# Optimization experiments

Hardware: AMD Instinct MI355X
Metric: run time of the kernel (lower is better)

Reference implementation:

```python
import jax, jax.numpy as jnp
import numpy as np

B, S, D, H = 2, 2048, 1024, 16
HD = D // H  # head dim = 64; scale uses sqrt(d_k/num_heads) = sqrt(D/H) since d_k==d_model


def setup_inputs() -> dict:
    key = jax.random.key(0)
    ks = jax.random.split(key, 12)
    s = 1.0 / np.sqrt(D)
    inp = {
        "Q": jax.random.normal(ks[0], (B, S, D), jnp.float32),
        "K": jax.random.normal(ks[1], (B, S, D), jnp.float32),
        "V": jax.random.normal(ks[2], (B, S, D), jnp.float32),
        "mask": jnp.tril(jnp.ones((S, S), jnp.int32))[None, None],  # [1,1,S,S] causal
        "Wq": jax.random.normal(ks[3], (D, D), jnp.float32) * s,
        "bq": jnp.zeros((D,), jnp.float32),
        "Wk": jax.random.normal(ks[4], (D, D), jnp.float32) * s,
        "bk": jnp.zeros((D,), jnp.float32),
        "Wv": jax.random.normal(ks[5], (D, D), jnp.float32) * s,
        "bv": jnp.zeros((D,), jnp.float32),
        "Wo": jax.random.normal(ks[6], (D, D), jnp.float32) * s,
        "bo": jnp.zeros((D,), jnp.float32),
    }
    return inp


def _split_heads(x):
    # [B,S,D] -> [B,H,S,HD]
    b, s, _ = x.shape
    return x.reshape(b, s, H, HD).transpose(0, 2, 1, 3)


def reference(Q, K, V, mask, Wq, bq, Wk, bk, Wv, bv, Wo, bo):
    q = _split_heads(Q @ Wq.T + bq)
    k = _split_heads(K @ Wk.T + bk)
    v = _split_heads(V @ Wv.T + bv)
    scale = 1.0 / jnp.sqrt(jnp.asarray(D / H, q.dtype))  # d_k/num_heads with d_k=d_model
    scores = jnp.einsum('bhqd,bhkd->bhqk', q, k) * scale
    scores = jnp.where(mask == 0, jnp.asarray(-1e9, scores.dtype), scores)
    probs = jax.nn.softmax(scores, axis=-1)
    z = jnp.einsum('bhqk,bhkd->bhqd', probs, v)  # [B,H,S,HD]
    z = z.transpose(0, 2, 1, 3).reshape(Q.shape[0], Q.shape[1], D)
    return z @ Wo.T + bo
```

## Files before the change

kernel.cpp:

```cpp
#include <hip/hip_runtime.h>
#include <hip/hip_bf16.h>

typedef unsigned short u16;
typedef unsigned int u32;
typedef __attribute__((ext_vector_type(8))) short s16x8;
typedef __attribute__((ext_vector_type(4))) float f32x4;
typedef __attribute__((ext_vector_type(16))) float f32x16;

#define NB 2
#define NH 16
#define NS 2048
#define ND 1024
#define QSCALE 0.1803368801111244f

#define AS1(p) ((const __attribute__((address_space(1))) void*)(p))
#define AS3(p) ((__attribute__((address_space(3))) void*)(p))

__device__ __forceinline__ u16 f2bf(float f) {
  u32 u = __float_as_uint(f);
  u = u + 0x7FFFu + ((u >> 16) & 1u);
  return (u16)(u >> 16);
}

__device__ __forceinline__ u32 pkbf(float a, float b) {
  __hip_bfloat162 h = __float22bfloat162_rn(make_float2(a, b));
  union { __hip_bfloat162 h; u32 u; } cv;
  cv.h = h;
  return cv.u;
}

__global__ __launch_bounds__(256) void cvt_kernel(
    const float* __restrict__ q, const float* __restrict__ k,
    const float* __restrict__ v, const float* __restrict__ wq,
    const float* __restrict__ wk, const float* __restrict__ wv,
    const float* __restrict__ wo, u16* __restrict__ Xbf,
    u16* __restrict__ Wbf) {
  const int z = blockIdx.z;
  const float* src;
  u16* dst;
  size_t n;
  const size_t NX = (size_t)4096 * 1024, NW = (size_t)1024 * 1024;
  if (z == 0)      { src = q;  dst = Xbf;          n = NX; }
  else if (z == 1) { src = k;  dst = Xbf + NX;     n = NX; }
  else if (z == 2) { src = v;  dst = Xbf + 2 * NX; n = NX; }
  else if (z == 3) { src = wq; dst = Wbf;          n = NW; }
  else if (z == 4) { src = wk; dst = Wbf + NW;     n = NW; }
  else if (z == 5) { src = wv; dst = Wbf + 2 * NW; n = NW; }
  else             { src = wo; dst = Wbf + 3 * NW; n = NW; }
  const size_t n4 = n >> 2;
  for (size_t i = (size_t)blockIdx.x * 256 + threadIdx.x; i < n4;
       i += (size_t)gridDim.x * 256) {
    float4 a = ((const float4*)src)[i];
    uint2 p;
    p.x = (u32)f2bf(a.x) | ((u32)f2bf(a.y) << 16);
    p.y = (u32)f2bf(a.z) | ((u32)f2bf(a.w) << 16);
    ((uint2*)dst)[i] = p;
  }
}

__global__ __launch_bounds__(256) void gemm_qkv_fast(
    const u16* __restrict__ Xbf, const u16* __restrict__ Wbf,
    const float* __restrict__ bq, const float* __restrict__ bk,
    const float* __restrict__ bv, u16* __restrict__ qh, u16* __restrict__ kh,
    u16* __restrict__ vT) {
  const int which = blockIdx.z;
  const u16* A = Xbf + (size_t)which * 4096 * 1024;
  const u16* B = Wbf + (size_t)which * 1024 * 1024;
  const float* bias = (which == 0) ? bq : (which == 1) ? bk : bv;
  const int m0 = blockIdx.y * 128, n0 = blockIdx.x * 128;
  const int tid = threadIdx.x;
  const int w = tid >> 6, l = tid & 63, lr = l & 15, lg = l >> 4;
  const int wr = (w >> 1) * 64, wc = (w & 1) * 64;

  __shared__ u16 As[128 * 32];
  __shared__ u16 Bs[128 * 32];

  const f32x4 fzero = {0.f, 0.f, 0.f, 0.f};
  f32x4 acc[4][4];
#pragma unroll
  for (int m = 0; m < 4; ++m)
#pragma unroll
    for (int n = 0; n < 4; ++n) acc[m][n] = fzero;

  for (int k0 = 0; k0 < 1024; k0 += 32) {
#pragma unroll
    for (int i = 0; i < 2; ++i) {
      int c = i * 256 + tid;
      int row = c >> 2, k4 = (c & 3) ^ (row & 3);
      const u16* sa = A + (size_t)(m0 + row) * 1024 + k0 + k4 * 8;
      const u16* sb = B + (size_t)(n0 + row) * 1024 + k0 + k4 * 8;
      u16* da = As + (i * 256 + w * 64) * 8;
      u16* db = Bs + (i * 256 + w * 64) * 8;
      __builtin_amdgcn_global_load_lds(AS1(sa), AS3(da), 16, 0, 0);
      __builtin_amdgcn_global_load_lds(AS1(sb), AS3(db), 16, 0, 0);
    }
    __syncthreads();
    s16x8 af[4], bf[4];
#pragma unroll
    for (int m = 0; m < 4; ++m) {
      int row = wr + m * 16 + lr;
      af[m] = *(const s16x8*)(As + row * 32 + ((lg ^ (row & 3)) * 8));
    }
#pragma unroll
    for (int n = 0; n < 4; ++n) {
      int row = wc + n * 16 + lr;
      bf[n] = *(const s16x8*)(Bs + row * 32 + ((lg ^ (row & 3)) * 8));
    }
#pragma unroll
    for (int m = 0; m < 4; ++m)
#pragma unroll
      for (int n = 0; n < 4; ++n)
        acc[m][n] = __builtin_amdgcn_mfma_f32_16x16x32_bf16(af[m], bf[n],
                                                            acc[m][n], 0, 0, 0);
    __syncthreads();
  }

#pragma unroll
  for (int m = 0; m < 4; ++m) {
#pragma unroll
    for (int n = 0; n < 4; ++n) {
#pragma unroll
      for (int i = 0; i < 4; ++i) {
        int row = m0 + wr + m * 16 + 4 * lg + i;
        int col = n0 + wc + n * 16 + lr;
        float val = acc[m][n][i] + bias[col];
        if (which == 0) val *= QSCALE;
        int bbi = row >> 11, ss = row & 2047;
        int hhd = col >> 6, hd = col & 63;
        if (which == 0) {
          qh[(((size_t)bbi * NH + hhd) * NS + ss) * 64 + hd] = f2bf(val);
        } else if (which == 1) {
          kh[(((size_t)bbi * NH + hhd) * NS + ss) * 64 + hd] = f2bf(val);
        } else {
          vT[(((size_t)bbi * NH + hhd) * 64 + hd) * NS + ss] = f2bf(val);
        }
      }
    }
  }
}

__global__ __launch_bounds__(256) void gemm_out_fast(
    const u16* __restrict__ zin, const u16* __restrict__ Wbf,
    const float* __restrict__ bo, float* __restrict__ out) {
  const u16* B = Wbf + (size_t)3 * 1024 * 1024;
  const int m0 = blockIdx.y * 128, n0 = blockIdx.x * 128;
  const int tid = threadIdx.x;
  const int w = tid >> 6, l = tid & 63, lr = l & 15, lg = l >> 4;
  const int wr = (w >> 1) * 64, wc = (w & 1) * 64;

  __shared__ u16 As[128 * 32];
  __shared__ u16 Bs[128 * 32];

  const f32x4 fzero = {0.f, 0.f, 0.f, 0.f};
  f32x4 acc[4][4];
#pragma unroll
  for (int m = 0; m < 4; ++m)
#pragma unroll
    for (int n = 0; n < 4; ++n) acc[m][n] = fzero;

  for (int k0 = 0; k0 < 1024; k0 += 32) {
#pragma unroll
    for (int i = 0; i < 2; ++i) {
      int c = i * 256 + tid;
      int row = c >> 2, k4 = (c & 3) ^ (row & 3);
      const u16* sa = zin + (size_t)(m0 + row) * 1024 + k0 + k4 * 8;
      const u16* sb = B + (size_t)(n0 + row) * 1024 + k0 + k4 * 8;
      u16* da = As + (i * 256 + w * 64) * 8;
      u16* db = Bs + (i * 256 + w * 64) * 8;
      __builtin_amdgcn_global_load_lds(AS1(sa), AS3(da), 16, 0, 0);
      __builtin_amdgcn_global_load_lds(AS1(sb), AS3(db), 16, 0, 0);
    }
    __syncthreads();
    s16x8 af[4], bf[4];
#pragma unroll
    for (int m = 0; m < 4; ++m) {
      int row = wr + m * 16 + lr;
      af[m] = *(const s16x8*)(As + row * 32 + ((lg ^ (row & 3)) * 8));
    }
#pragma unroll
    for (int n = 0; n < 4; ++n) {
      int row = wc + n * 16 + lr;
      bf[n] = *(const s16x8*)(Bs + row * 32 + ((lg ^ (row & 3)) * 8));
    }
#pragma unroll
    for (int m = 0; m < 4; ++m)
#pragma unroll
      for (int n = 0; n < 4; ++n)
        acc[m][n] = __builtin_amdgcn_mfma_f32_16x16x32_bf16(af[m], bf[n],
                                                            acc[m][n], 0, 0, 0);
    __syncthreads();
  }

#pragma unroll
  for (int m = 0; m < 4; ++m)
#pragma unroll
    for (int n = 0; n < 4; ++n)
#pragma unroll
      for (int i = 0; i < 4; ++i) {
        int row = m0 + wr + m * 16 + 4 * lg + i;
        int col = n0 + wc + n * 16 + lr;
        out[(size_t)row * 1024 + col] = acc[m][n][i] + bo[col];
      }
}

__global__ __launch_bounds__(256) void proj_qkv_kernel(
    const float* __restrict__ Qin, const float* __restrict__ Kin,
    const float* __restrict__ Vin,
    const float* __restrict__ Wq, const float* __restrict__ bq,
    const float* __restrict__ Wk, const float* __restrict__ bk,
    const float* __restrict__ Wv, const float* __restrict__ bv,
    u16* __restrict__ qh, u16* __restrict__ kh, u16* __restrict__ vT) {
  const int which = blockIdx.z;
  const float* X = (which == 0) ? Qin : (which == 1) ? Kin : Vin;
  const float* W = (which == 0) ? Wq : (which == 1) ? Wk : Wv;
  const float* bias = (which == 0) ? bq : (which == 1) ? bk : bv;

  const int m0 = blockIdx.y * 128, n0 = blockIdx.x * 128;
  const int tid = threadIdx.x;
  const int w = tid >> 6, l = tid & 63, lr = l & 15, lg = l >> 4;
  const int wr = (w >> 1) * 64, wc = (w & 1) * 64;

  __shared__ u16 As[128][40];
  __shared__ u16 Bs[128][40];

  const f32x4 fzero = {0.f, 0.f, 0.f, 0.f};
  f32x4 acc[4][4];
#pragma unroll
  for (int m = 0; m < 4; ++m)
#pragma unroll
    for (int n = 0; n < 4; ++n) acc[m][n] = fzero;

  for (int k0 = 0; k0 < 1024; k0 += 32) {
#pragma unroll
    for (int i = 0; i < 4; ++i) {
      int idx = tid + i * 256;
      int row = idx >> 3, c4 = (idx & 7) * 4;
      float4 a = *(const float4*)(X + (size_t)(m0 + row) * 1024 + k0 + c4);
      *(u32*)&As[row][c4]     = (u32)f2bf(a.x) | ((u32)f2bf(a.y) << 16);
      *(u32*)&As[row][c4 + 2] = (u32)f2bf(a.z) | ((u32)f2bf(a.w) << 16);
      float4 b = *(const float4*)(W + (size_t)(n0 + row) * 1024 + k0 + c4);
      *(u32*)&Bs[row][c4]     = (u32)f2bf(b.x) | ((u32)f2bf(b.y) << 16);
      *(u32*)&Bs[row][c4 + 2] = (u32)f2bf(b.z) | ((u32)f2bf(b.w) << 16);
    }
    __syncthreads();
    s16x8 af[4], bf[4];
#pragma unroll
    for (int m = 0; m < 4; ++m)
      af[m] = *(const s16x8*)&As[wr + m * 16 + lr][lg * 8];
#pragma unroll
    for (int n = 0; n < 4; ++n)
      bf[n] = *(const s16x8*)&Bs[wc + n * 16 + lr][lg * 8];
#pragma unroll
    for (int m = 0; m < 4; ++m)
#pragma unroll
      for (int n = 0; n < 4; ++n)
        acc[m][n] = __builtin_amdgcn_mfma_f32_16x16x32_bf16(af[m], bf[n],
                                                            acc[m][n], 0, 0, 0);
    __syncthreads();
  }

  u16* dst01 = (which == 0) ? qh : kh;
#pragma unroll
  for (int m = 0; m < 4; ++m) {
#pragma unroll
    for (int n = 0; n < 4; ++n) {
#pragma unroll
      for (int i = 0; i < 4; ++i) {
        int row = m0 + wr + m * 16 + 4 * lg + i;
        int col = n0 + wc + n * 16 + lr;
        float val = acc[m][n][i] + bias[col];
        if (which == 0) val *= QSCALE;
        int bbi = row >> 11, ss = row & 2047;
        int hhd = col >> 6, hd = col & 63;
        if (which < 2) {
          dst01[(((size_t)bbi * NH + hhd) * NS + ss) * 64 + hd] = f2bf(val);
        } else {
          vT[(((size_t)bbi * NH + hhd) * 64 + hd) * NS + ss] = f2bf(val);
        }
      }
    }
  }
}

__global__ __launch_bounds__(256) void proj_out_kernel(
    const u16* __restrict__ zin, const float* __restrict__ Wo,
    const float* __restrict__ bo, float* __restrict__ out) {
  const int m0 = blockIdx.y * 128, n0 = blockIdx.x * 128;
  const int tid = threadIdx.x;
  const int w = tid >> 6, l = tid & 63, lr = l & 15, lg = l >> 4;
  const int wr = (w >> 1) * 64, wc = (w & 1) * 64;

  __shared__ u16 As[128][40];
  __shared__ u16 Bs[128][40];

  const f32x4 fzero = {0.f, 0.f, 0.f, 0.f};
  f32x4 acc[4][4];
#pragma unroll
  for (int m = 0; m < 4; ++m)
#pragma unroll
    for (int n = 0; n < 4; ++n) acc[m][n] = fzero;

  for (int k0 = 0; k0 < 1024; k0 += 32) {
#pragma unroll
    for (int i = 0; i < 2; ++i) {
      int idx = tid + i * 256;
      int row = idx >> 2, c8 = (idx & 3) * 8;
      *(s16x8*)&As[row][c8] =
          *(const s16x8*)(zin + (size_t)(m0 + row) * 1024 + k0 + c8);
    }
#pragma unroll
    for (int i = 0; i < 4; ++i) {
      int idx = tid + i * 256;
      int row = idx >> 3, c4 = (idx & 7) * 4;
      float4 b = *(const float4*)(Wo + (size_t)(n0 + row) * 1024 + k0 + c4);
      *(u32*)&Bs[row][c4]     = (u32)f2bf(b.x) | ((u32)f2bf(b.y) << 16);
      *(u32*)&Bs[row][c4 + 2] = (u32)f2bf(b.z) | ((u32)f2bf(b.w) << 16);
    }
    __syncthreads();
    s16x8 af[4], bf[4];
#pragma unroll
    for (int m = 0; m < 4; ++m)
      af[m] = *(const s16x8*)&As[wr + m * 16 + lr][lg * 8];
#pragma unroll
    for (int n = 0; n < 4; ++n)
      bf[n] = *(const s16x8*)&Bs[wc + n * 16 + lr][lg * 8];
#pragma unroll
    for (int m = 0; m < 4; ++m)
#pragma unroll
      for (int n = 0; n < 4; ++n)
        acc[m][n] = __builtin_amdgcn_mfma_f32_16x16x32_bf16(af[m], bf[n],
                                                            acc[m][n], 0, 0, 0);
    __syncthreads();
  }

#pragma unroll
  for (int m = 0; m < 4; ++m)
#pragma unroll
    for (int n = 0; n < 4; ++n)
#pragma unroll
      for (int i = 0; i < 4; ++i) {
        int row = m0 + wr + m * 16 + 4 * lg + i;
        int col = n0 + wc + n * 16 + lr;
        out[(size_t)row * 1024 + col] = acc[m][n][i] + bo[col];
      }
}

__global__ __launch_bounds__(256) void attn_kernel(
    const u16* __restrict__ qh, const u16* __restrict__ kh,
    const u16* __restrict__ vT, u16* __restrict__ z) {
  const int f = blockIdx.x;
  const int bh = f & 31;
  const int j = f >> 5;
  const int qb = (j < 8) ? (15 - j) : (j - 8);
  const int bb = bh >> 4, hh = bh & 15;
  const int tid = threadIdx.x;
  const int w = tid >> 6, l = tid & 63;
  const int ql = l & 31, hi = l >> 5, hi8 = hi * 8;
  const int q0b = qb * 128;
  const int q0w = q0b + w * 32;

  __shared__ u16 smem[2][2][64][64];

  s16x8 qf[4];
  {
    const u16* qp = qh + ((size_t)bh * NS + q0w + ql) * 64 + hi8;
#pragma unroll
    for (int st = 0; st < 4; ++st) qf[st] = *(const s16x8*)(qp + st * 16);
  }

  f32x16 o0 = {0, 0, 0, 0, 0, 0, 0, 0, 0, 0, 0, 0, 0, 0, 0, 0};
  f32x16 o1 = {0, 0, 0, 0, 0, 0, 0, 0, 0, 0, 0, 0, 0, 0, 0, 0};
  float m_run = -1e30f, l_run = 0.f;

  const int ntiles = (q0b + 128) >> 6;

#pragma unroll
  for (int i = 0; i < 2; ++i) {
    int c = i * 256 + tid;
    int row = c >> 3, k8 = (c & 7) ^ (row & 7);
    const u16* sk = kh + ((size_t)bh * NS + row) * 64 + k8 * 8;
    const u16* sv = vT + ((size_t)bh * 64 + row) * NS + k8 * 8;
    u16* dk = &smem[0][0][0][0] + (i * 256 + w * 64) * 8;
    u16* dv = &smem[0][1][0][0] + (i * 256 + w * 64) * 8;
    __builtin_amdgcn_global_load_lds(AS1(sk), AS3(dk), 16, 0, 0);
    __builtin_amdgcn_global_load_lds(AS1(sv), AS3(dv), 16, 0, 0);
  }
  __syncthreads();

  for (int t = 0; t < ntiles; ++t) {
    if (t + 1 < ntiles) {
      int b1 = (t + 1) & 1;
#pragma unroll
      for (int i = 0; i < 2; ++i) {
        int c = i * 256 + tid;
        int row = c >> 3, k8 = (c & 7) ^ (row & 7);
        const u16* sk =
            kh + ((size_t)bh * NS + (t + 1) * 64 + row) * 64 + k8 * 8;
        const u16* sv =
            vT + ((size_t)bh * 64 + row) * NS + (t + 1) * 64 + k8 * 8;
        u16* dk = &smem[b1][0][0][0] + (i * 256 + w * 64) * 8;
        u16* dv = &smem[b1][1][0][0] + (i * 256 + w * 64) * 8;
        __builtin_amdgcn_global_load_lds(AS1(sk), AS3(dk), 16, 0, 0);
        __builtin_amdgcn_global_load_lds(AS1(sv), AS3(dv), 16, 0, 0);
      }
    }
    const u16* kp = &smem[t & 1][0][0][0];
    const u16* vp = &smem[t & 1][1][0][0];

#pragma unroll
    for (int sub = 0; sub < 2; ++sub) {
      const int kvg = t * 64 + sub * 32;
      if (kvg > q0w) continue;
      const bool masked = (kvg == q0w);

      const int kr = sub * 32 + ql;
      f32x16 s = {0, 0, 0, 0, 0, 0, 0, 0, 0, 0, 0, 0, 0, 0, 0, 0};
#pragma unroll
      for (int st = 0; st < 4; ++st) {
        s16x8 ak = *(const s16x8*)(kp + kr * 64 +
                                   (((st * 2 + hi) ^ (kr & 7)) * 8));
        s = __builtin_amdgcn_mfma_f32_32x32x16_bf16(ak, qf[st], s, 0, 0, 0);
      }

      float sv_[16];
#pragma unroll
      for (int r = 0; r < 16; ++r) {
        float x = s[r];
        if (masked) {
          int kvloc = (r & 3) + 8 * (r >> 2) + 4 * hi;
          if (kvloc > ql) x = -1e30f;
        }
        sv_[r] = x;
      }

      float mx = sv_[0];
#pragma unroll
      for (int r = 1; r < 16; ++r) mx = fmaxf(mx, sv_[r]);
      mx = fmaxf(mx, __shfl_xor(mx, 32, 64));

      if (__any(mx > m_run)) {
        float mnew = fmaxf(m_run, mx);
        float fs = __builtin_amdgcn_exp2f(m_run - mnew);
#pragma unroll
        for (int r = 0; r < 16; ++r) {
          o0[r] *= fs;
          o1[r] *= fs;
        }
        l_run *= fs;
        m_run = mnew;
      }

      float ps = 0.f;
      u32 pk[8];
#pragma unroll
      for (int tt = 0; tt < 8; ++tt) {
        float a = __builtin_amdgcn_exp2f(sv_[2 * tt] - m_run);
        float b = __builtin_amdgcn_exp2f(sv_[2 * tt + 1] - m_run);
        ps += a + b;
        pk[tt] = pkbf(a, b);
      }
      ps += __shfl_xor(ps, 32, 64);
      l_run += ps;

      u32 qk[8];
#pragma unroll
      for (int tt = 0; tt < 8; ++tt) qk[tt] = __shfl_xor(pk[tt], 32, 64);

      union { u32 u[4]; s16x8 h; } pf0, pf1;
      pf0.u[0] = hi ? qk[2] : pk[0];
      pf0.u[1] = hi ? qk[3] : pk[1];
      pf0.u[2] = hi ? pk[2] : qk[0];
      pf0.u[3] = hi ? pk[3] : qk[1];
      pf1.u[0] = hi ? qk[6] : pk[4];
      pf1.u[1] = hi ? qk[7] : pk[5];
      pf1.u[2] = hi ? pk[6] : qk[4];
      pf1.u[3] = hi ? pk[7] : qk[5];

#pragma unroll
      for (int k2 = 0; k2 < 2; ++k2) {
        s16x8 pa = (k2 == 0) ? pf0.h : pf1.h;
        int ch = sub * 4 + k2 * 2 + hi;
        s16x8 av0 = *(const s16x8*)(vp + ql * 64 + ((ch ^ (ql & 7)) * 8));
        s16x8 av1 =
            *(const s16x8*)(vp + (32 + ql) * 64 + ((ch ^ (ql & 7)) * 8));
        o0 = __builtin_amdgcn_mfma_f32_32x32x16_bf16(av0, pa, o0, 0, 0, 0);
        o1 = __builtin_amdgcn_mfma_f32_32x32x16_bf16(av1, pa, o1, 0, 0, 0);
      }
    }
    __syncthreads();
  }

  float inv = 1.f / l_run;
  u16* Zw = &smem[0][0][0][0] + w * (32 * 72);
#pragma unroll
  for (int r = 0; r < 16; r += 2) {
    int d0 = (r & 3) + 8 * (r >> 2) + 4 * hi;
    *(u32*)&Zw[ql * 72 + d0]      = pkbf(o0[r] * inv, o0[r + 1] * inv);
    *(u32*)&Zw[ql * 72 + 32 + d0] = pkbf(o1[r] * inv, o1[r + 1] * inv);
  }
#pragma unroll
  for (int i = 0; i < 4; ++i) {
    int cid = i * 64 + l;
    int row = cid >> 3, c8 = (cid & 7) * 8;
    s16x8 vv = *(const s16x8*)&Zw[row * 72 + c8];
    *(s16x8*)(z + ((size_t)bb * NS + q0w + row) * ND + hh * 64 + c8) = vv;
  }
}

extern "C" void kernel_launch(void* const* d_in, const int* in_sizes, int n_in,
                              void* d_out, int out_size, void* d_ws,
                              size_t ws_size, hipStream_t stream) {
  const float* Q = (const float*)d_in[0];
  const float* K = (const float*)d_in[1];
  const float* V = (const float*)d_in[2];
  const float* Wq = (const float*)d_in[4];
  const float* bq = (const float*)d_in[5];
  const float* Wk = (const float*)d_in[6];
  const float* bk = (const float*)d_in[7];
  const float* Wv = (const float*)d_in[8];
  const float* bv = (const float*)d_in[9];
  const float* Wo = (const float*)d_in[10];
  const float* bo = (const float*)d_in[11];
  float* out = (float*)d_out;

  const size_t M1 = (size_t)1024 * 1024;
  u16* base = (u16*)d_ws;

  if (ws_size >= (size_t)58720256) {
    u16* Wbf = base;
    u16* qh = base + 4 * M1;
    u16* kh = base + 8 * M1;
    u16* vT = base + 12 * M1;
    u16* Xbf = base + 16 * M1;
    u16* zz = base + 16 * M1;

    cvt_kernel<<<dim3(512, 1, 7), 256, 0, stream>>>(Q, K, V, Wq, Wk, Wv, Wo,
                                                    Xbf, Wbf);
    gemm_qkv_fast<<<dim3(8, 32, 3), 256, 0, stream>>>(Xbf, Wbf, bq, bk, bv, qh,
                                                      kh, vT);
    attn_kernel<<<dim3(512), 256, 0, stream>>>(qh, kh, vT, zz);
    gemm_out_fast<<<dim3(8, 32), 256, 0, stream>>>(zz, Wbf, bo, out);
  } else {
    u16* qh = base;
    u16* kh = base + 4 * M1;
    u16* vT = base + 8 * M1;
    u16* zz = base + 12 * M1;
    proj_qkv_kernel<<<dim3(8, 32, 3), 256, 0, stream>>>(Q, K, V, Wq, bq, Wk,
                                                        bk, Wv, bv, qh, kh, vT);
    attn_kernel<<<dim3(512), 256, 0, stream>>>(qh, kh, vT, zz);
    proj_out_kernel<<<dim3(8, 32), 256, 0, stream>>>(zz, Wo, bo, out);
  }
}
```

Measured before the change: 148.9 us.

## Shrink attention blocks to 64 query rows, balance causal work, use permlane32 swaps

The attention kernel now runs 1024 blocks of 128 threads, each covering 64 query rows instead of 128. Block-to-query mapping is interleaved so each group of blocks pairs short and long causal rows for load balance. Cross-half-wave reductions and the P-fragment exchange now use permlane32_swap instead of shfl_xor plus selects, and s_setprio raises priority around the MFMA sections. Smaller blocks raise occupancy and parallelism, but each 64-row block reloads the full K/V prefix, so K/V traffic per query roughly doubles.

Result: slower. 160.9 us (+8.1%).

```diff
diff --git a/kernel.cpp b/kernel.cpp
--- a/kernel.cpp
+++ b/kernel.cpp
@@ -3,6 +3,7 @@
 
 typedef unsigned short u16;
 typedef unsigned int u32;
+typedef __attribute__((ext_vector_type(2))) unsigned int u32x2;
 typedef __attribute__((ext_vector_type(8))) short s16x8;
 typedef __attribute__((ext_vector_type(4))) float f32x4;
 typedef __attribute__((ext_vector_type(16))) float f32x16;
@@ -203,6 +204,176 @@
       }
 }
 
+__global__ __launch_bounds__(128) void attn_kernel(
+    const u16* __restrict__ qh, const u16* __restrict__ kh,
+    const u16* __restrict__ vT, u16* __restrict__ z) {
+  const int f = blockIdx.x;
+  const int bh = f & 31;
+  const int j0 = (f >> 5) & 7;
+  const int g = f >> 8;
+  const int mb = 2 * j0;
+  const int m =
+      (g == 0) ? mb : (g == 1) ? mb + 1 : (g == 2) ? 30 - mb : 31 - mb;
+  const int bb = bh >> 4, hh = bh & 15;
+  const int tid = threadIdx.x;
+  const int w = tid >> 6, l = tid & 63;
+  const int ql = l & 31, hi = l >> 5, hi8 = hi * 8;
+  const int q0w = m * 64 + w * 32;
+
+  __shared__ u16 smem[2][2][64][64];
+
+  s16x8 qf[4];
+  {
+    const u16* qp = qh + ((size_t)bh * NS + q0w + ql) * 64 + hi8;
+#pragma unroll
+    for (int st = 0; st < 4; ++st) qf[st] = *(const s16x8*)(qp + st * 16);
+  }
+
+  f32x16 o0 = {0, 0, 0, 0, 0, 0, 0, 0, 0, 0, 0, 0, 0, 0, 0, 0};
+  f32x16 o1 = {0, 0, 0, 0, 0, 0, 0, 0, 0, 0, 0, 0, 0, 0, 0, 0};
+  float m_run = -1e30f, l_run = 0.f;
+
+  const int ntiles = m + 1;
+
+#pragma unroll
+  for (int i = 0; i < 4; ++i) {
+    int c = i * 128 + tid;
+    int row = c >> 3, k8 = (c & 7) ^ (row & 7);
+    const u16* sk = kh + ((size_t)bh * NS + row) * 64 + k8 * 8;
+    const u16* sv = vT + ((size_t)bh * 64 + row) * NS + k8 * 8;
+    u16* dk = &smem[0][0][0][0] + (i * 128 + w * 64) * 8;
+    u16* dv = &smem[0][1][0][0] + (i * 128 + w * 64) * 8;
+    __builtin_amdgcn_global_load_lds(AS1(sk), AS3(dk), 16, 0, 0);
+    __builtin_amdgcn_global_load_lds(AS1(sv), AS3(dv), 16, 0, 0);
+  }
+  __syncthreads();
+
+  for (int t = 0; t < ntiles; ++t) {
+    if (t + 1 < ntiles) {
+      int b1 = (t + 1) & 1;
+#pragma unroll
+      for (int i = 0; i < 4; ++i) {
+        int c = i * 128 + tid;
+        int row = c >> 3, k8 = (c & 7) ^ (row & 7);
+        const u16* sk =
+            kh + ((size_t)bh * NS + (t + 1) * 64 + row) * 64 + k8 * 8;
+        const u16* sv =
+            vT + ((size_t)bh * 64 + row) * NS + (t + 1) * 64 + k8 * 8;
+        u16* dk = &smem[b1][0][0][0] + (i * 128 + w * 64) * 8;
+        u16* dv = &smem[b1][1][0][0] + (i * 128 + w * 64) * 8;
+        __builtin_amdgcn_global_load_lds(AS1(sk), AS3(dk), 16, 0, 0);
+        __builtin_amdgcn_global_load_lds(AS1(sv), AS3(dv), 16, 0, 0);
+      }
+    }
+    const u16* kp = &smem[t & 1][0][0][0];
+    const u16* vp = &smem[t & 1][1][0][0];
+
+#pragma unroll
+    for (int sub = 0; sub < 2; ++sub) {
+      const int kvg = t * 64 + sub * 32;
+      if (kvg > q0w) continue;
+      const bool masked = (kvg == q0w);
+
+      const int kr = sub * 32 + ql;
+      f32x16 s = {0, 0, 0, 0, 0, 0, 0, 0, 0, 0, 0, 0, 0, 0, 0, 0};
+      __builtin_amdgcn_s_setprio(1);
+#pragma unroll
+      for (int st = 0; st < 4; ++st) {
+        s16x8 ak = *(const s16x8*)(kp + kr * 64 +
+                                   (((st * 2 + hi) ^ (kr & 7)) * 8));
+        s = __builtin_amdgcn_mfma_f32_32x32x16_bf16(ak, qf[st], s, 0, 0, 0);
+      }
+      __builtin_amdgcn_s_setprio(0);
+
+      float sv_[16];
+#pragma unroll
+      for (int r = 0; r < 16; ++r) {
+        float x = s[r];
+        if (masked) {
+          int kvloc = (r & 3) + 8 * (r >> 2) + 4 * hi;
+          if (kvloc > ql) x = -1e30f;
+        }
+        sv_[r] = x;
+      }
+
+      float mx = sv_[0];
+#pragma unroll
+      for (int r = 1; r < 16; ++r) mx = fmaxf(mx, sv_[r]);
+      {
+        u32x2 rm = __builtin_amdgcn_permlane32_swap(__float_as_uint(mx),
+                                                    __float_as_uint(mx), 0, 0);
+        mx = fmaxf(__uint_as_float(rm.x), __uint_as_float(rm.y));
+      }
+
+      if (__any(mx > m_run)) {
+        float mnew = fmaxf(m_run, mx);
+        float fs = __builtin_amdgcn_exp2f(m_run - mnew);
+#pragma unroll
+        for (int r = 0; r < 16; ++r) {
+          o0[r] *= fs;
+          o1[r] *= fs;
+        }
+        l_run *= fs;
+        m_run = mnew;
+      }
+
+      float ps = 0.f;
+      u32 pk[8];
+#pragma unroll
+      for (int tt = 0; tt < 8; ++tt) {
+        float a = __builtin_amdgcn_exp2f(sv_[2 * tt] - m_run);
+        float b = __builtin_amdgcn_exp2f(sv_[2 * tt + 1] - m_run);
+        ps += a + b;
+        pk[tt] = pkbf(a, b);
+      }
+      {
+        u32x2 rp = __builtin_amdgcn_permlane32_swap(__float_as_uint(ps),
+                                                    __float_as_uint(ps), 0, 0);
+        ps = __uint_as_float(rp.x) + __uint_as_float(rp.y);
+      }
+      l_run += ps;
+
+      u32x2 e0 = __builtin_amdgcn_permlane32_swap(pk[0], pk[2], 0, 0);
+      u32x2 e1 = __builtin_amdgcn_permlane32_swap(pk[1], pk[3], 0, 0);
+      u32x2 e2 = __builtin_amdgcn_permlane32_swap(pk[4], pk[6], 0, 0);
+      u32x2 e3 = __builtin_amdgcn_permlane32_swap(pk[5], pk[7], 0, 0);
+      union { u32 u[4]; s16x8 h; } pf0, pf1;
+      pf0.u[0] = e0.x; pf0.u[1] = e1.x; pf0.u[2] = e0.y; pf0.u[3] = e1.y;
+      pf1.u[0] = e2.x; pf1.u[1] = e3.x; pf1.u[2] = e2.y; pf1.u[3] = e3.y;
+
+      __builtin_amdgcn_s_setprio(1);
+#pragma unroll
+      for (int k2 = 0; k2 < 2; ++k2) {
+        s16x8 pa = (k2 == 0) ? pf0.h : pf1.h;
+        int ch = sub * 4 + k2 * 2 + hi;
+        s16x8 av0 = *(const s16x8*)(vp + ql * 64 + ((ch ^ (ql & 7)) * 8));
+        s16x8 av1 =
+            *(const s16x8*)(vp + (32 + ql) * 64 + ((ch ^ (ql & 7)) * 8));
+        o0 = __builtin_amdgcn_mfma_f32_32x32x16_bf16(av0, pa, o0, 0, 0, 0);
+        o1 = __builtin_amdgcn_mfma_f32_32x32x16_bf16(av1, pa, o1, 0, 0, 0);
+      }
+      __builtin_amdgcn_s_setprio(0);
+    }
+    __syncthreads();
+  }
+
+  float inv = 1.f / l_run;
+  u16* Zw = &smem[0][0][0][0] + w * (32 * 72);
+#pragma unroll
+  for (int r = 0; r < 16; r += 2) {
+    int d0 = (r & 3) + 8 * (r >> 2) + 4 * hi;
+    *(u32*)&Zw[ql * 72 + d0]      = pkbf(o0[r] * inv, o0[r + 1] * inv);
+    *(u32*)&Zw[ql * 72 + 32 + d0] = pkbf(o1[r] * inv, o1[r + 1] * inv);
+  }
+#pragma unroll
+  for (int i = 0; i < 4; ++i) {
+    int cid = i * 64 + l;
+    int row = cid >> 3, c8 = (cid & 7) * 8;
+    s16x8 vv = *(const s16x8*)&Zw[row * 72 + c8];
+    *(s16x8*)(z + ((size_t)bb * NS + q0w + row) * ND + hh * 64 + c8) = vv;
+  }
+}
+
 __global__ __launch_bounds__(256) void proj_qkv_kernel(
     const float* __restrict__ Qin, const float* __restrict__ Kin,
     const float* __restrict__ Vin,
@@ -343,168 +514,6 @@
         int col = n0 + wc + n * 16 + lr;
         out[(size_t)row * 1024 + col] = acc[m][n][i] + bo[col];
       }
-}
-
-__global__ __launch_bounds__(256) void attn_kernel(
-    const u16* __restrict__ qh, const u16* __restrict__ kh,
-    const u16* __restrict__ vT, u16* __restrict__ z) {
-  const int f = blockIdx.x;
-  const int bh = f & 31;
-  const int j = f >> 5;
-  const int qb = (j < 8) ? (15 - j) : (j - 8);
-  const int bb = bh >> 4, hh = bh & 15;
-  const int tid = threadIdx.x;
-  const int w = tid >> 6, l = tid & 63;
-  const int ql = l & 31, hi = l >> 5, hi8 = hi * 8;
-  const int q0b = qb * 128;
-  const int q0w = q0b + w * 32;
-
-  __shared__ u16 smem[2][2][64][64];
-
-  s16x8 qf[4];
-  {
-    const u16* qp = qh + ((size_t)bh * NS + q0w + ql) * 64 + hi8;
-#pragma unroll
-    for (int st = 0; st < 4; ++st) qf[st] = *(const s16x8*)(qp + st * 16);
-  }
-
-  f32x16 o0 = {0, 0, 0, 0, 0, 0, 0, 0, 0, 0, 0, 0, 0, 0, 0, 0};
-  f32x16 o1 = {0, 0, 0, 0, 0, 0, 0, 0, 0, 0, 0, 0, 0, 0, 0, 0};
-  float m_run = -1e30f, l_run = 0.f;
-
-  const int ntiles = (q0b + 128) >> 6;
-
-#pragma unroll
-  for (int i = 0; i < 2; ++i) {
-    int c = i * 256 + tid;
-    int row = c >> 3, k8 = (c & 7) ^ (row & 7);
-    const u16* sk = kh + ((size_t)bh * NS + row) * 64 + k8 * 8;
-    const u16* sv = vT + ((size_t)bh * 64 + row) * NS + k8 * 8;
-    u16* dk = &smem[0][0][0][0] + (i * 256 + w * 64) * 8;
-    u16* dv = &smem[0][1][0][0] + (i * 256 + w * 64) * 8;
-    __builtin_amdgcn_global_load_lds(AS1(sk), AS3(dk), 16, 0, 0);
-    __builtin_amdgcn_global_load_lds(AS1(sv), AS3(dv), 16, 0, 0);
-  }
-  __syncthreads();
-
-  for (int t = 0; t < ntiles; ++t) {
-    if (t + 1 < ntiles) {
-      int b1 = (t + 1) & 1;
-#pragma unroll
-      for (int i = 0; i < 2; ++i) {
-        int c = i * 256 + tid;
-        int row = c >> 3, k8 = (c & 7) ^ (row & 7);
-        const u16* sk =
-            kh + ((size_t)bh * NS + (t + 1) * 64 + row) * 64 + k8 * 8;
-        const u16* sv =
-            vT + ((size_t)bh * 64 + row) * NS + (t + 1) * 64 + k8 * 8;
-        u16* dk = &smem[b1][0][0][0] + (i * 256 + w * 64) * 8;
-        u16* dv = &smem[b1][1][0][0] + (i * 256 + w * 64) * 8;
-        __builtin_amdgcn_global_load_lds(AS1(sk), AS3(dk), 16, 0, 0);
-        __builtin_amdgcn_global_load_lds(AS1(sv), AS3(dv), 16, 0, 0);
-      }
-    }
-    const u16* kp = &smem[t & 1][0][0][0];
-    const u16* vp = &smem[t & 1][1][0][0];
-
-#pragma unroll
-    for (int sub = 0; sub < 2; ++sub) {
-      const int kvg = t * 64 + sub * 32;
-      if (kvg > q0w) continue;
-      const bool masked = (kvg == q0w);
-
-      const int kr = sub * 32 + ql;
-      f32x16 s = {0, 0, 0, 0, 0, 0, 0, 0, 0, 0, 0, 0, 0, 0, 0, 0};
-#pragma unroll
-      for (int st = 0; st < 4; ++st) {
-        s16x8 ak = *(const s16x8*)(kp + kr * 64 +
-                                   (((st * 2 + hi) ^ (kr & 7)) * 8));
-        s = __builtin_amdgcn_mfma_f32_32x32x16_bf16(ak, qf[st], s, 0, 0, 0);
-      }
-
-      float sv_[16];
-#pragma unroll
-      for (int r = 0; r < 16; ++r) {
-        float x = s[r];
-        if (masked) {
-          int kvloc = (r & 3) + 8 * (r >> 2) + 4 * hi;
-          if (kvloc > ql) x = -1e30f;
-        }
-        sv_[r] = x;
-      }
-
-      float mx = sv_[0];
-#pragma unroll
-      for (int r = 1; r < 16; ++r) mx = fmaxf(mx, sv_[r]);
-      mx = fmaxf(mx, __shfl_xor(mx, 32, 64));
-
-      if (__any(mx > m_run)) {
-        float mnew = fmaxf(m_run, mx);
-        float fs = __builtin_amdgcn_exp2f(m_run - mnew);
-#pragma unroll
-        for (int r = 0; r < 16; ++r) {
-          o0[r] *= fs;
-          o1[r] *= fs;
-        }
-        l_run *= fs;
-        m_run = mnew;
-      }
-
-      float ps = 0.f;
-      u32 pk[8];
-#pragma unroll
-      for (int tt = 0; tt < 8; ++tt) {
-        float a = __builtin_amdgcn_exp2f(sv_[2 * tt] - m_run);
-        float b = __builtin_amdgcn_exp2f(sv_[2 * tt + 1] - m_run);
-        ps += a + b;
-        pk[tt] = pkbf(a, b);
-      }
-      ps += __shfl_xor(ps, 32, 64);
-      l_run += ps;
-
-      u32 qk[8];
-#pragma unroll
-      for (int tt = 0; tt < 8; ++tt) qk[tt] = __shfl_xor(pk[tt], 32, 64);
-
-      union { u32 u[4]; s16x8 h; } pf0, pf1;
-      pf0.u[0] = hi ? qk[2] : pk[0];
-      pf0.u[1] = hi ? qk[3] : pk[1];
-      pf0.u[2] = hi ? pk[2] : qk[0];
-      pf0.u[3] = hi ? pk[3] : qk[1];
-      pf1.u[0] = hi ? qk[6] : pk[4];
-      pf1.u[1] = hi ? qk[7] : pk[5];
-      pf1.u[2] = hi ? pk[6] : qk[4];
-      pf1.u[3] = hi ? pk[7] : qk[5];
-
-#pragma unroll
-      for (int k2 = 0; k2 < 2; ++k2) {
-        s16x8 pa = (k2 == 0) ? pf0.h : pf1.h;
-        int ch = sub * 4 + k2 * 2 + hi;
-        s16x8 av0 = *(const s16x8*)(vp + ql * 64 + ((ch ^ (ql & 7)) * 8));
-        s16x8 av1 =
-            *(const s16x8*)(vp + (32 + ql) * 64 + ((ch ^ (ql & 7)) * 8));
-        o0 = __builtin_amdgcn_mfma_f32_32x32x16_bf16(av0, pa, o0, 0, 0, 0);
-        o1 = __builtin_amdgcn_mfma_f32_32x32x16_bf16(av1, pa, o1, 0, 0, 0);
-      }
-    }
-    __syncthreads();
-  }
-
-  float inv = 1.f / l_run;
-  u16* Zw = &smem[0][0][0][0] + w * (32 * 72);
-#pragma unroll
-  for (int r = 0; r < 16; r += 2) {
-    int d0 = (r & 3) + 8 * (r >> 2) + 4 * hi;
-    *(u32*)&Zw[ql * 72 + d0]      = pkbf(o0[r] * inv, o0[r + 1] * inv);
-    *(u32*)&Zw[ql * 72 + 32 + d0] = pkbf(o1[r] * inv, o1[r + 1] * inv);
-  }
-#pragma unroll
-  for (int i = 0; i < 4; ++i) {
-    int cid = i * 64 + l;
-    int row = cid >> 3, c8 = (cid & 7) * 8;
-    s16x8 vv = *(const s16x8*)&Zw[row * 72 + c8];
-    *(s16x8*)(z + ((size_t)bb * NS + q0w + row) * ND + hh * 64 + c8) = vv;
-  }
 }
 
 extern "C" void kernel_launch(void* const* d_in, const int* in_sizes, int n_in,
@@ -538,7 +547,7 @@
                                                     Xbf, Wbf);
     gemm_qkv_fast<<<dim3(8, 32, 3), 256, 0, stream>>>(Xbf, Wbf, bq, bk, bv, qh,
                                                       kh, vT);
-    attn_kernel<<<dim3(512), 256, 0, stream>>>(qh, kh, vT, zz);
+    attn_kernel<<<dim3(1024), 128, 0, stream>>>(qh, kh, vT, zz);
     gemm_out_fast<<<dim3(8, 32), 256, 0, stream>>>(zz, Wbf, bo, out);
   } else {
     u16* qh = base;
@@ -547,7 +556,7 @@
     u16* zz = base + 12 * M1;
     proj_qkv_kernel<<<dim3(8, 32, 3), 256, 0, stream>>>(Q, K, V, Wq, bq, Wk,
                                                         bk, Wv, bv, qh, kh, vT);
-    attn_kernel<<<dim3(512), 256, 0, stream>>>(qh, kh, vT, zz);
+    attn_kernel<<<dim3(1024), 128, 0, stream>>>(qh, kh, vT, zz);
     proj_out_kernel<<<dim3(8, 32), 256, 0, stream>>>(zz, Wo, bo, out);
   }
 }
```
